# Optimization experiments

Measured on AMD Instinct MI355X. Metric: run time of the kernel, lower is better.

Reference implementation:

```python
import jax, jax.numpy as jnp
import numpy as np

MAT_MODE = [(0, 1), (0, 2), (1, 2)]   # plane axes per component (TensoRF VM)
VEC_MODE = [2, 1, 0]                  # line axis per component
DISTANCE_SCALE = 1.0
WHITE_BG = True


def _bilinear(plane, uv):
    """plane: [C,H,W]; uv: [P,2] in [-1,1] (uv[:,0]->W, uv[:,1]->H). align_corners=True."""
    H, W = plane.shape[-2], plane.shape[-1]
    x = (uv[:, 0] + 1.0) * 0.5 * (W - 1)
    y = (uv[:, 1] + 1.0) * 0.5 * (H - 1)
    x0 = jnp.clip(jnp.floor(x), 0, W - 2).astype(jnp.int32)
    y0 = jnp.clip(jnp.floor(y), 0, H - 2).astype(jnp.int32)
    wx = x - x0
    wy = y - y0
    v00 = plane[:, y0, x0]
    v01 = plane[:, y0, x0 + 1]
    v10 = plane[:, y0 + 1, x0]
    v11 = plane[:, y0 + 1, x0 + 1]
    top = v00 * (1 - wx) + v01 * wx
    bot = v10 * (1 - wx) + v11 * wx
    return top * (1 - wy) + bot * wy   # [C,P]


def _linear1d(line, t):
    """line: [C,L]; t: [P] in [-1,1]. align_corners=True."""
    L = line.shape[-1]
    x = (t + 1.0) * 0.5 * (L - 1)
    x0 = jnp.clip(jnp.floor(x), 0, L - 2).astype(jnp.int32)
    w = x - x0
    return line[:, x0] * (1 - w) + line[:, x0 + 1] * w   # [C,P]


def setup_inputs() -> dict:
    key = jax.random.key(0)
    ks = jax.random.split(key, 8)
    N_rays = 4096
    # camera origins on a sphere of radius 4, dirs aimed at points inside the box
    o = jax.random.normal(ks[0], (N_rays, 3), jnp.float32)
    o = o / jnp.linalg.norm(o, axis=-1, keepdims=True) * 4.0
    tgt = jax.random.uniform(ks[1], (N_rays, 3), jnp.float32, -0.5, 0.5)
    d = tgt - o
    d = d / jnp.linalg.norm(d, axis=-1, keepdims=True)
    rays = jnp.concatenate([o, d], axis=-1)
    return {
        "rays": rays,
        "density_plane": 0.1 * jax.random.normal(ks[2], (3, 16, 256, 256), jnp.float32),
        "density_line": 0.1 * jax.random.normal(ks[3], (3, 16, 256), jnp.float32),
        "app_plane": 0.1 * jax.random.normal(ks[4], (3, 24, 256, 256), jnp.float32),
        "app_line": 0.1 * jax.random.normal(ks[5], (3, 24, 256), jnp.float32),
        "basis_mat": 0.1 * jax.random.normal(ks[6], (72, 3), jnp.float32),
        "aabb": jnp.array([[-1.5, -1.5, -1.5], [1.5, 1.5, 1.5]], jnp.float32),
        "N_samples": 256,
    }


def reference(rays, density_plane, density_line, app_plane, app_line, basis_mat, aabb, N_samples):
    N = rays.shape[0]
    o, d = rays[:, :3], rays[:, 3:6]
    # ray / aabb intersection
    vec = jnp.where(jnp.abs(d) < 1e-6, 1e-6, d)
    rate_a = (aabb[1] - o) / vec
    rate_b = (aabb[0] - o) / vec
    t_min = jnp.clip(jnp.minimum(rate_a, rate_b).max(-1), 0.05)
    t_max = jnp.maximum(jnp.maximum(rate_a, rate_b).min(-1), t_min + 1e-3)
    s = jnp.linspace(0.0, 1.0, N_samples, dtype=jnp.float32)
    z = t_min[:, None] * (1.0 - s) + t_max[:, None] * s          # [N,S]
    dists = jnp.diff(z, axis=-1)
    dists = jnp.concatenate([dists, dists[:, -1:]], axis=-1)      # [N,S]
    pts = o[:, None, :] + d[:, None, :] * z[..., None]            # [N,S,3]
    coords = (pts - aabb[0]) / (aabb[1] - aabb[0]) * 2.0 - 1.0
    inside = jnp.all(jnp.abs(coords) <= 1.0, axis=-1)             # [N,S]
    cf = coords.reshape(-1, 3)                                    # [P,3]

    sigma_feat = 0.0
    app_feats = []
    for i in range(3):
        uv = cf[:, list(MAT_MODE[i])]
        w = cf[:, VEC_MODE[i]]
        sigma_feat = sigma_feat + (_bilinear(density_plane[i], uv) * _linear1d(density_line[i], w)).sum(0)
        app_feats.append(_bilinear(app_plane[i], uv) * _linear1d(app_line[i], w))
    app = jnp.concatenate(app_feats, axis=0).T                    # [P, 72]

    sigma = jax.nn.softplus(sigma_feat).reshape(N, -1) * inside   # [N,S]
    alpha = 1.0 - jnp.exp(-sigma * dists * DISTANCE_SCALE)        # [N,S]
    T = jnp.cumprod(1.0 - alpha + 1e-10, axis=-1)
    T = jnp.concatenate([jnp.ones_like(T[:, :1]), T[:, :-1]], axis=-1)
    weights = alpha * T                                           # [N,S]

    rgb = jax.nn.sigmoid(app @ basis_mat).reshape(N, -1, 3)       # [N,S,3]
    rgb_map = (weights[..., None] * rgb).sum(1)                   # [N,3]
    acc = weights.sum(-1)
    if WHITE_BG:
        rgb_map = rgb_map + (1.0 - acc)[..., None]
    rgb_map = jnp.clip(rgb_map, 0.0, 1.0)
    depth_map = (weights * z).sum(-1, keepdims=True)              # [N,1]
    return rgb_map, depth_map
```

## Files before the change

### kernel.cpp

```cpp
#include <hip/hip_runtime.h>
#include <hip/hip_fp16.h>
#include <cmath>

#define NRAYS 4096
#define NSAMP 256
#define NSAMPLES_TOT (NRAYS * NSAMP)

static constexpr size_t DPT_B = 0;
static constexpr size_t DLT_B = 6291456;
static constexpr size_t APT_B = DLT_B + 24576;
static constexpr size_t ALT_B = APT_B + 6291456;
static constexpr size_t SMP_B = ALT_B + 24576;
static constexpr size_t RAY_B = SMP_B + 8388608;
static constexpr size_t WS_NEED = RAY_B + 131072;

typedef _Float16 __attribute__((ext_vector_type(2))) v2h;
typedef __attribute__((ext_vector_type(2))) float f32x2;

__device__ __forceinline__ float dot2acc(__half2 a, __half2 b, float c) {
  return __builtin_amdgcn_fdot2(__builtin_bit_cast(v2h, a),
                                __builtin_bit_cast(v2h, b), c, false);
}

__device__ __forceinline__ __half2 lerp2(__half2 a, __half2 b, __half2 w) {
  return __hfma2(w, __hsub2(b, a), a);
}

__device__ __forceinline__ void ld8h(const __half* p, __half2 h[4]) {
  uint4 r = *(const uint4*)p;
  h[0] = __builtin_bit_cast(__half2, r.x);
  h[1] = __builtin_bit_cast(__half2, r.y);
  h[2] = __builtin_bit_cast(__half2, r.z);
  h[3] = __builtin_bit_cast(__half2, r.w);
}

__device__ __forceinline__ unsigned pack2h(float a, float b) {
  return __builtin_bit_cast(unsigned, __floats2half2_rn(a, b));
}

__device__ __forceinline__ void dec4f8h(unsigned w, __half2& h0, __half2& h1) {
  f32x2 lo = __builtin_amdgcn_cvt_pk_f32_fp8((int)w, false);
  f32x2 hi = __builtin_amdgcn_cvt_pk_f32_fp8((int)w, true);
  h0 = __floats2half2_rn(lo.x, lo.y);
  h1 = __floats2half2_rn(hi.x, hi.y);
}

__device__ __forceinline__ void dec16f8(uint4 q, __half2 h[8]) {
  dec4f8h(q.x, h[0], h[1]);
  dec4f8h(q.y, h[2], h[3]);
  dec4f8h(q.z, h[4], h[5]);
  dec4f8h(q.w, h[6], h[7]);
}

__device__ __forceinline__ unsigned pk4f8(float a, float b, float c, float d) {
  int w = __builtin_amdgcn_cvt_pk_fp8_f32(a, b, 0, false);
  w = __builtin_amdgcn_cvt_pk_fp8_f32(c, d, w, true);
  return (unsigned)w;
}

__device__ __forceinline__ void grid_uv(float c, int& i0, float& w) {
  float f = (c + 1.0f) * 127.5f;
  float fl = floorf(f);
  fl = fminf(fmaxf(fl, 0.0f), 254.0f);
  i0 = (int)fl;
  w = f - fl;
}

__global__ __launch_bounds__(256) void prep_kernel(
    const float* __restrict__ dp, const float* __restrict__ ap,
    const float* __restrict__ dl, const float* __restrict__ al,
    const float* __restrict__ rays, const float* __restrict__ aabb,
    __half* __restrict__ dpt, unsigned char* __restrict__ apt,
    __half* __restrict__ dlt, unsigned char* __restrict__ alt,
    float4* __restrict__ rd) {
  __shared__ float tile[24][257];
  int b = blockIdx.x, x = threadIdx.x;
  if (b < 768) {
    int i = b >> 8, y = b & 255;
    const float* src = dp + (size_t)(i * 16) * 65536 + y * 256;
#pragma unroll
    for (int c = 0; c < 16; ++c) tile[c][x] = src[c * 65536 + x];
    __syncthreads();
    float f[16];
#pragma unroll
    for (int c = 0; c < 16; ++c) f[c] = tile[c][x];
    uint4 v0, v1;
    v0.x = pack2h(f[0], f[1]);   v0.y = pack2h(f[2], f[3]);
    v0.z = pack2h(f[4], f[5]);   v0.w = pack2h(f[6], f[7]);
    v1.x = pack2h(f[8], f[9]);   v1.y = pack2h(f[10], f[11]);
    v1.z = pack2h(f[12], f[13]); v1.w = pack2h(f[14], f[15]);
    uint4* dst = (uint4*)(dpt + ((size_t)(i << 16) + (y << 8) + x) * 16);
    dst[0] = v0; dst[1] = v1;
  } else if (b < 1536) {
    int t = b - 768;
    int i = t >> 8, y = t & 255;
    const float* src = ap + (size_t)(i * 24) * 65536 + y * 256;
#pragma unroll
    for (int c = 0; c < 24; ++c) tile[c][x] = src[c * 65536 + x];
    __syncthreads();
    float f[24];
#pragma unroll
    for (int c = 0; c < 24; ++c) f[c] = tile[c][x];
    uint4 v0, v1;
    v0.x = pk4f8(f[0], f[1], f[2], f[3]);
    v0.y = pk4f8(f[4], f[5], f[6], f[7]);
    v0.z = pk4f8(f[8], f[9], f[10], f[11]);
    v0.w = pk4f8(f[12], f[13], f[14], f[15]);
    v1.x = pk4f8(f[16], f[17], f[18], f[19]);
    v1.y = pk4f8(f[20], f[21], f[22], f[23]);
    v1.z = 0u; v1.w = 0u;
    uint4* dst = (uint4*)(apt + ((size_t)(i << 16) + (y << 8) + x) * 32);
    dst[0] = v0; dst[1] = v1;
  } else if (b < 1539) {
    int i = b - 1536, l = x;
    float f[16];
#pragma unroll
    for (int c = 0; c < 16; ++c) f[c] = dl[(i * 16 + c) * 256 + l];
    uint4 v0, v1;
    v0.x = pack2h(f[0], f[1]);   v0.y = pack2h(f[2], f[3]);
    v0.z = pack2h(f[4], f[5]);   v0.w = pack2h(f[6], f[7]);
    v1.x = pack2h(f[8], f[9]);   v1.y = pack2h(f[10], f[11]);
    v1.z = pack2h(f[12], f[13]); v1.w = pack2h(f[14], f[15]);
    uint4* dst = (uint4*)(dlt + (i * 256 + l) * 16);
    dst[0] = v0; dst[1] = v1;
  } else if (b < 1542) {
    int i = b - 1539, l = x;
    float f[24];
#pragma unroll
    for (int c = 0; c < 24; ++c) f[c] = al[(i * 24 + c) * 256 + l];
    uint4 v0, v1;
    v0.x = pk4f8(f[0], f[1], f[2], f[3]);
    v0.y = pk4f8(f[4], f[5], f[6], f[7]);
    v0.z = pk4f8(f[8], f[9], f[10], f[11]);
    v0.w = pk4f8(f[12], f[13], f[14], f[15]);
    v1.x = pk4f8(f[16], f[17], f[18], f[19]);
    v1.y = pk4f8(f[20], f[21], f[22], f[23]);
    v1.z = 0u; v1.w = 0u;
    uint4* dst = (uint4*)(alt + (i * 256 + l) * 32);
    dst[0] = v0; dst[1] = v1;
  } else {
    int r = (b - 1542) * 256 + x;
    if (r < NRAYS) {
      float o0 = rays[r * 6 + 0], o1 = rays[r * 6 + 1], o2 = rays[r * 6 + 2];
      float d0 = rays[r * 6 + 3], d1 = rays[r * 6 + 4], d2 = rays[r * 6 + 5];
      float A0 = aabb[0], A1 = aabb[1], A2 = aabb[2];
      float B0 = aabb[3], B1 = aabb[4], B2 = aabb[5];
      float v0 = fabsf(d0) < 1e-6f ? 1e-6f : d0;
      float v1 = fabsf(d1) < 1e-6f ? 1e-6f : d1;
      float v2 = fabsf(d2) < 1e-6f ? 1e-6f : d2;
      float ra0 = (B0 - o0) / v0, rb0 = (A0 - o0) / v0;
      float ra1 = (B1 - o1) / v1, rb1 = (A1 - o1) / v1;
      float ra2 = (B2 - o2) / v2, rb2 = (A2 - o2) / v2;
      float tmin = fmaxf(fmaxf(fminf(ra0, rb0), fminf(ra1, rb1)), fminf(ra2, rb2));
      tmin = fmaxf(tmin, 0.05f);
      float tmax = fminf(fminf(fmaxf(ra0, rb0), fmaxf(ra1, rb1)), fmaxf(ra2, rb2));
      tmax = fmaxf(tmax, tmin + 0.001f);
      float dt = (tmax - tmin) * (1.0f / 255.0f);
      float s0 = 2.0f / (B0 - A0), s1 = 2.0f / (B1 - A1), s2 = 2.0f / (B2 - A2);
      float4 a2, b2;
      a2.x = (o0 - A0) * s0 - 1.0f; a2.y = (o1 - A1) * s1 - 1.0f;
      a2.z = (o2 - A2) * s2 - 1.0f; a2.w = tmin;
      b2.x = d0 * s0; b2.y = d1 * s1; b2.z = d2 * s2; b2.w = dt;
      rd[r * 2] = a2;
      rd[r * 2 + 1] = b2;
    }
  }
}

__device__ __forceinline__ float density_h2(const __half* __restrict__ pl,
                                            const __half* __restrict__ ln,
                                            int x0, __half2 wx, int y0, __half2 wy,
                                            int l0, __half2 wl, int sub,
                                            float acc) {
  const __half* p = pl + ((y0 * 256 + x0) << 4) + sub * 8;
  __half2 v00[4], v01[4], v10[4], v11[4], la[4], lb[4];
  ld8h(p, v00);
  ld8h(p + 16, v01);
  ld8h(p + 4096, v10);
  ld8h(p + 4096 + 16, v11);
  const __half* lp = ln + (l0 << 4) + sub * 8;
  ld8h(lp, la);
  ld8h(lp + 16, lb);
#pragma unroll
  for (int r = 0; r < 4; ++r) {
    __half2 m = lerp2(lerp2(v00[r], v01[r], wx), lerp2(v10[r], v11[r], wx), wy);
    __half2 l = lerp2(la[r], lb[r], wl);
    acc = dot2acc(m, l, acc);
  }
  return acc;
}

__device__ __forceinline__ void app_f8(const unsigned char* __restrict__ pl,
                                       const unsigned char* __restrict__ ln,
                                       const __half2* __restrict__ btR,
                                       const __half2* __restrict__ btG,
                                       const __half2* __restrict__ btB,
                                       int x0, __half2 wx, int y0, __half2 wy,
                                       int l0, __half2 wl, int sub,
                                       float& dr, float& dg, float& db) {
  const unsigned char* p = pl + (size_t)((y0 * 256 + x0) << 5) + sub * 16;
  uint4 qA = *(const uint4*)p;
  uint4 qB = *(const uint4*)(p + 32);
  uint4 qC = *(const uint4*)(p + 8192);
  uint4 qD = *(const uint4*)(p + 8192 + 32);
  const unsigned char* lp = ln + (l0 << 5) + sub * 16;
  uint4 qLA = *(const uint4*)lp;
  uint4 qLB = *(const uint4*)(lp + 32);
  __half2 A[8], B[8], C[8], D[8], LA[8], LB[8];
  dec16f8(qA, A);
  dec16f8(qB, B);
  dec16f8(qC, C);
  dec16f8(qD, D);
  dec16f8(qLA, LA);
  dec16f8(qLB, LB);
#pragma unroll
  for (int r = 0; r < 8; ++r) {
    __half2 m = lerp2(lerp2(A[r], B[r], wx), lerp2(C[r], D[r], wx), wy);
    __half2 l = lerp2(LA[r], LB[r], wl);
    __half2 av = __hmul2(m, l);
    dr = dot2acc(av, btR[r], dr);
    dg = dot2acc(av, btG[r], dg);
    db = dot2acc(av, btB[r], db);
  }
}

__global__ __launch_bounds__(256) void sample_kernel(
    const float4* __restrict__ rd, const float* __restrict__ basis,
    const __half* __restrict__ dpt, const __half* __restrict__ dlt,
    const unsigned char* __restrict__ apt, const unsigned char* __restrict__ alt,
    uint2* __restrict__ smp) {
  __shared__ __align__(16) __half bth[3][3][32];
  int tid = threadIdx.x;
  for (int t = tid; t < 288; t += 256) {
    int k = t / 96, rem = t - k * 96;
    int m = rem >> 5, c = rem & 31;
    float v = (c < 24) ? basis[(m * 24 + c) * 3 + k] : 0.0f;
    bth[k][m][c] = __float2half(v);
  }
  __syncthreads();

  int ray = blockIdx.x >> 1;
  int j = ((blockIdx.x & 1) << 7) + (tid >> 1);
  int sub = tid & 1;

  float4 ra = rd[ray * 2];
  float4 rb = rd[ray * 2 + 1];
  float z = fmaf((float)j, rb.w, ra.w);
  float c0 = fmaf(rb.x, z, ra.x);
  float c1 = fmaf(rb.y, z, ra.y);
  float c2 = fmaf(rb.z, z, ra.z);
  bool inside = (fabsf(c0) <= 1.0f) && (fabsf(c1) <= 1.0f) && (fabsf(c2) <= 1.0f);

  float sig = 0.f, dr = 0.f, dg = 0.f, db = 0.f;
  if (inside) {
    int i0, i1, i2;
    float w0, w1, w2;
    grid_uv(c0, i0, w0);
    grid_uv(c1, i1, w1);
    grid_uv(c2, i2, w2);
    __half2 h0 = __float2half2_rn(w0);
    __half2 h1 = __float2half2_rn(w1);
    __half2 h2 = __float2half2_rn(w2);
    sig = density_h2(dpt + 0 * 1048576, dlt + 0 * 4096, i0, h0, i1, h1, i2, h2, sub, sig);
    sig = density_h2(dpt + 1 * 1048576, dlt + 1 * 4096, i0, h0, i2, h2, i1, h1, sub, sig);
    sig = density_h2(dpt + 2 * 1048576, dlt + 2 * 4096, i1, h1, i2, h2, i0, h0, sub, sig);
    app_f8(apt + 0 * 2097152, alt + 0 * 8192,
           (const __half2*)&bth[0][0][sub * 16], (const __half2*)&bth[1][0][sub * 16],
           (const __half2*)&bth[2][0][sub * 16], i0, h0, i1, h1, i2, h2, sub, dr, dg, db);
    app_f8(apt + 1 * 2097152, alt + 1 * 8192,
           (const __half2*)&bth[0][1][sub * 16], (const __half2*)&bth[1][1][sub * 16],
           (const __half2*)&bth[2][1][sub * 16], i0, h0, i2, h2, i1, h1, sub, dr, dg, db);
    app_f8(apt + 2 * 2097152, alt + 2 * 8192,
           (const __half2*)&bth[0][2][sub * 16], (const __half2*)&bth[1][2][sub * 16],
           (const __half2*)&bth[2][2][sub * 16], i1, h1, i2, h2, i0, h0, sub, dr, dg, db);
  }
  sig += __shfl_xor(sig, 1, 64);
  dr += __shfl_xor(dr, 1, 64);
  dg += __shfl_xor(dg, 1, 64);
  db += __shfl_xor(db, 1, 64);

  if (sub == 0) {
    float sp = fmaxf(sig, 0.f) + log1pf(expf(-fabsf(sig)));
    float alpha = inside ? (1.0f - expf(-sp * rb.w)) : 0.0f;
    float cr = 1.0f / (1.0f + expf(-dr));
    float cg = 1.0f / (1.0f + expf(-dg));
    float cb = 1.0f / (1.0f + expf(-db));
    uint2 sv;
    sv.x = pack2h(alpha, cr);
    sv.y = pack2h(cg, cb);
    smp[ray * 256 + j] = sv;
  }
}

__global__ __launch_bounds__(256) void scan_kernel(
    const float4* __restrict__ rd, const uint2* __restrict__ smp,
    float* __restrict__ out) {
  int tid = threadIdx.x;
  int lane = tid & 63;
  int ray = blockIdx.x * 4 + (tid >> 6);

  float tmin = rd[ray * 2].w;
  float dt = rd[ray * 2 + 1].w;

  float C = 1.0f;
  float racc = 0.f, gacc = 0.f, bacc = 0.f, wsum = 0.f, dsum = 0.f;

  for (int q = 0; q < 4; ++q) {
    int j = q * 64 + lane;
    uint2 sv = smp[ray * 256 + j];
    float2 ar = __half22float2(__builtin_bit_cast(__half2, sv.x));
    float2 gb = __half22float2(__builtin_bit_cast(__half2, sv.y));
    float alpha = ar.x;
    float z = fmaf((float)j, dt, tmin);

    float p = 1.0f - alpha + 1e-10f;
#pragma unroll
    for (int off = 1; off < 64; off <<= 1) {
      float t = __shfl_up(p, off, 64);
      if (lane >= off) p *= t;
    }
    float tot = __shfl(p, 63, 64);
    float e = __shfl_up(p, 1, 64);
    if (lane == 0) e = 1.0f;
    float Tj = C * e;
    float w = alpha * Tj;
    racc += w * ar.y;
    gacc += w * gb.x;
    bacc += w * gb.y;
    wsum += w;
    dsum += w * z;
    C *= tot;
  }

#pragma unroll
  for (int off = 32; off > 0; off >>= 1) {
    racc += __shfl_down(racc, off, 64);
    gacc += __shfl_down(gacc, off, 64);
    bacc += __shfl_down(bacc, off, 64);
    wsum += __shfl_down(wsum, off, 64);
    dsum += __shfl_down(dsum, off, 64);
  }
  if (lane == 0) {
    float bgw = 1.0f - wsum;
    out[ray * 3 + 0] = fminf(fmaxf(racc + bgw, 0.f), 1.f);
    out[ray * 3 + 1] = fminf(fmaxf(gacc + bgw, 0.f), 1.f);
    out[ray * 3 + 2] = fminf(fmaxf(bacc + bgw, 0.f), 1.f);
    out[NRAYS * 3 + ray] = dsum;
  }
}

__device__ __forceinline__ float density_orig(const float* __restrict__ plane,
                                              const float* __restrict__ line,
                                              float cx, float cy, float cw) {
  int x0, y0, l0; float wx, wy, wl;
  grid_uv(cx, x0, wx); grid_uv(cy, y0, wy); grid_uv(cw, l0, wl);
  int base = y0 * 256 + x0;
  float s = 0.0f;
#pragma unroll 4
  for (int c = 0; c < 16; ++c) {
    const float* pc = plane + c * 65536;
    float v00 = pc[base], v01 = pc[base + 1];
    float v10 = pc[base + 256], v11 = pc[base + 257];
    float top = fmaf(wx, v01 - v00, v00);
    float bot = fmaf(wx, v11 - v10, v10);
    float mid = fmaf(wy, bot - top, top);
    float la = line[c * 256 + l0], lb = line[c * 256 + l0 + 1];
    float lv = fmaf(wl, lb - la, la);
    s += mid * lv;
  }
  return s;
}

__device__ __forceinline__ void app_orig(const float* __restrict__ plane,
                                         const float* __restrict__ line,
                                         const float* __restrict__ btR,
                                         const float* __restrict__ btG,
                                         const float* __restrict__ btB,
                                         float cx, float cy, float cw,
                                         float& dr, float& dg, float& db) {
  int x0, y0, l0; float wx, wy, wl;
  grid_uv(cx, x0, wx); grid_uv(cy, y0, wy); grid_uv(cw, l0, wl);
  int base = y0 * 256 + x0;
#pragma unroll 4
  for (int c = 0; c < 24; ++c) {
    const float* pc = plane + c * 65536;
    float v00 = pc[base], v01 = pc[base + 1];
    float v10 = pc[base + 256], v11 = pc[base + 257];
    float top = fmaf(wx, v01 - v00, v00);
    float bot = fmaf(wx, v11 - v10, v10);
    float mid = fmaf(wy, bot - top, top);
    float la = line[c * 256 + l0], lb = line[c * 256 + l0 + 1];
    float lv = fmaf(wl, lb - la, la);
    float av = mid * lv;
    dr += av * btR[c]; dg += av * btG[c]; db += av * btB[c];
  }
}

__global__ __launch_bounds__(256) void render_fallback(
    const float* __restrict__ rays, const float* __restrict__ basis,
    const float* __restrict__ aabb, const float* __restrict__ dplane,
    const float* __restrict__ dline, const float* __restrict__ aplane,
    const float* __restrict__ aline, float* __restrict__ out) {
  __shared__ float bt[3 * 72];
  int tid = threadIdx.x;
  if (tid < 216) {
    int k = tid / 72, r = tid - k * 72;
    bt[tid] = basis[r * 3 + k];
  }
  __syncthreads();
  int lane = tid & 63;
  int ray = blockIdx.x * 4 + (tid >> 6);

  float o0 = rays[ray * 6 + 0], o1 = rays[ray * 6 + 1], o2 = rays[ray * 6 + 2];
  float d0 = rays[ray * 6 + 3], d1 = rays[ray * 6 + 4], d2 = rays[ray * 6 + 5];
  float A0 = aabb[0], A1 = aabb[1], A2 = aabb[2];
  float B0 = aabb[3], B1 = aabb[4], B2 = aabb[5];
  float v0 = fabsf(d0) < 1e-6f ? 1e-6f : d0;
  float v1 = fabsf(d1) < 1e-6f ? 1e-6f : d1;
  float v2 = fabsf(d2) < 1e-6f ? 1e-6f : d2;
  float ra0 = (B0 - o0) / v0, rb0 = (A0 - o0) / v0;
  float ra1 = (B1 - o1) / v1, rb1 = (A1 - o1) / v1;
  float ra2 = (B2 - o2) / v2, rb2 = (A2 - o2) / v2;
  float tmin = fmaxf(fmaxf(fminf(ra0, rb0), fminf(ra1, rb1)), fminf(ra2, rb2));
  tmin = fmaxf(tmin, 0.05f);
  float tmax = fminf(fminf(fmaxf(ra0, rb0), fmaxf(ra1, rb1)), fmaxf(ra2, rb2));
  tmax = fmaxf(tmax, tmin + 0.001f);
  float dt = (tmax - tmin) * (1.0f / 255.0f);
  float s0 = 2.0f / (B0 - A0), s1 = 2.0f / (B1 - A1), s2 = 2.0f / (B2 - A2);

  float C = 1.0f;
  float racc = 0.f, gacc = 0.f, bacc = 0.f, wsum = 0.f, dsum = 0.f;
  for (int q = 0; q < 4; ++q) {
    int j = q * 64 + lane;
    float sfrac = (float)j * (1.0f / 255.0f);
    float z = tmin * (1.0f - sfrac) + tmax * sfrac;
    float c0 = (o0 + d0 * z - A0) * s0 - 1.0f;
    float c1 = (o1 + d1 * z - A1) * s1 - 1.0f;
    float c2 = (o2 + d2 * z - A2) * s2 - 1.0f;
    bool inside = (fabsf(c0) <= 1.0f) && (fabsf(c1) <= 1.0f) && (fabsf(c2) <= 1.0f);
    float alpha = 0.f, cr = 0.f, cg = 0.f, cb = 0.f;
    if (inside) {
      float sig = 0.f, dr = 0.f, dg = 0.f, db = 0.f;
      sig += density_orig(dplane + 0 * 1048576, dline + 0 * 4096, c0, c1, c2);
      sig += density_orig(dplane + 1 * 1048576, dline + 1 * 4096, c0, c2, c1);
      sig += density_orig(dplane + 2 * 1048576, dline + 2 * 4096, c1, c2, c0);
      app_orig(aplane + 0 * 1572864, aline + 0 * 6144,
               &bt[0 * 72 + 0], &bt[1 * 72 + 0], &bt[2 * 72 + 0],
               c0, c1, c2, dr, dg, db);
      app_orig(aplane + 1 * 1572864, aline + 1 * 6144,
               &bt[0 * 72 + 24], &bt[1 * 72 + 24], &bt[2 * 72 + 24],
               c0, c2, c1, dr, dg, db);
      app_orig(aplane + 2 * 1572864, aline + 2 * 6144,
               &bt[0 * 72 + 48], &bt[1 * 72 + 48], &bt[2 * 72 + 48],
               c1, c2, c0, dr, dg, db);
      float sp = fmaxf(sig, 0.f) + log1pf(expf(-fabsf(sig)));
      alpha = 1.0f - expf(-sp * dt);
      cr = 1.0f / (1.0f + expf(-dr));
      cg = 1.0f / (1.0f + expf(-dg));
      cb = 1.0f / (1.0f + expf(-db));
    }
    float p = 1.0f - alpha + 1e-10f;
#pragma unroll
    for (int off = 1; off < 64; off <<= 1) {
      float t = __shfl_up(p, off, 64);
      if (lane >= off) p *= t;
    }
    float tot = __shfl(p, 63, 64);
    float e = __shfl_up(p, 1, 64);
    if (lane == 0) e = 1.0f;
    float Tj = C * e;
    float w = alpha * Tj;
    racc += w * cr; gacc += w * cg; bacc += w * cb;
    wsum += w; dsum += w * z;
    C *= tot;
  }
#pragma unroll
  for (int off = 32; off > 0; off >>= 1) {
    racc += __shfl_down(racc, off, 64);
    gacc += __shfl_down(gacc, off, 64);
    bacc += __shfl_down(bacc, off, 64);
    wsum += __shfl_down(wsum, off, 64);
    dsum += __shfl_down(dsum, off, 64);
  }
  if (lane == 0) {
    float bgw = 1.0f - wsum;
    out[ray * 3 + 0] = fminf(fmaxf(racc + bgw, 0.f), 1.f);
    out[ray * 3 + 1] = fminf(fmaxf(gacc + bgw, 0.f), 1.f);
    out[ray * 3 + 2] = fminf(fmaxf(bacc + bgw, 0.f), 1.f);
    out[NRAYS * 3 + ray] = dsum;
  }
}

extern "C" void kernel_launch(void* const* d_in, const int* in_sizes, int n_in,
                              void* d_out, int out_size, void* d_ws, size_t ws_size,
                              hipStream_t stream) {
  const float* rays  = (const float*)d_in[0];
  const float* dp    = (const float*)d_in[1];
  const float* dl    = (const float*)d_in[2];
  const float* ap    = (const float*)d_in[3];
  const float* al    = (const float*)d_in[4];
  const float* basis = (const float*)d_in[5];
  const float* aabb  = (const float*)d_in[6];
  float* out = (float*)d_out;

  if (ws_size >= WS_NEED) {
    char* ws = (char*)d_ws;
    __half* dpt = (__half*)(ws + DPT_B);
    __half* dlt = (__half*)(ws + DLT_B);
    unsigned char* apt = (unsigned char*)(ws + APT_B);
    unsigned char* alt = (unsigned char*)(ws + ALT_B);
    uint2* smp = (uint2*)(ws + SMP_B);
    float4* rayd = (float4*)(ws + RAY_B);
    prep_kernel<<<1558, 256, 0, stream>>>(dp, ap, dl, al, rays, aabb,
                                          dpt, apt, dlt, alt, rayd);
    sample_kernel<<<NRAYS * 2, 256, 0, stream>>>(rayd, basis, dpt, dlt, apt, alt, smp);
    scan_kernel<<<NRAYS / 4, 256, 0, stream>>>(rayd, smp, out);
  } else {
    render_fallback<<<NRAYS / 4, 256, 0, stream>>>(
        rays, basis, aabb, dp, dl, ap, al, out);
  }
}
```

Measured before the change: 171.2 us.

## Store density planes in fp8, drop app padding, precompute bilinear weights

Density plane tables are quantized from fp16 to fp8, which halves their footprint. Appearance plane and line tables are packed at 24 bytes per texel instead of a padded 32, cutting the gather bytes per sample. Bilinear interpolation now uses four precomputed corner weights per plane, each shared by the density and appearance lookups, instead of nested lerps. In exchange the density features lose precision, and the 12-byte unaligned loads may split into several smaller memory instructions.

```diff
diff --git a/kernel.cpp b/kernel.cpp
--- a/kernel.cpp
+++ b/kernel.cpp
@@ -7,15 +7,23 @@
 #define NSAMPLES_TOT (NRAYS * NSAMP)
 
 static constexpr size_t DPT_B = 0;
-static constexpr size_t DLT_B = 6291456;
+static constexpr size_t DLT_B = 3145728;
 static constexpr size_t APT_B = DLT_B + 24576;
-static constexpr size_t ALT_B = APT_B + 6291456;
-static constexpr size_t SMP_B = ALT_B + 24576;
+static constexpr size_t ALT_B = APT_B + 4718592;
+static constexpr size_t SMP_B = ALT_B + 18432;
 static constexpr size_t RAY_B = SMP_B + 8388608;
 static constexpr size_t WS_NEED = RAY_B + 131072;
 
 typedef _Float16 __attribute__((ext_vector_type(2))) v2h;
 typedef __attribute__((ext_vector_type(2))) float f32x2;
+
+struct u96 { unsigned x, y, z; };
+
+__device__ __forceinline__ u96 ld12(const void* p) {
+  u96 v;
+  __builtin_memcpy(&v, p, 12);
+  return v;
+}
 
 __device__ __forceinline__ float dot2acc(__half2 a, __half2 b, float c) {
   return __builtin_amdgcn_fdot2(__builtin_bit_cast(v2h, a),
@@ -45,11 +53,15 @@
   h1 = __floats2half2_rn(hi.x, hi.y);
 }
 
-__device__ __forceinline__ void dec16f8(uint4 q, __half2 h[8]) {
+__device__ __forceinline__ void dec8f8(uint2 q, __half2 h[4]) {
+  dec4f8h(q.x, h[0], h[1]);
+  dec4f8h(q.y, h[2], h[3]);
+}
+
+__device__ __forceinline__ void dec12f8(u96 q, __half2 h[6]) {
   dec4f8h(q.x, h[0], h[1]);
   dec4f8h(q.y, h[2], h[3]);
   dec4f8h(q.z, h[4], h[5]);
-  dec4f8h(q.w, h[6], h[7]);
 }
 
 __device__ __forceinline__ unsigned pk4f8(float a, float b, float c, float d) {
@@ -66,11 +78,20 @@
   w = f - fl;
 }
 
+__device__ __forceinline__ void bilin_w(float wx, float wy, __half2& W00,
+                                        __half2& W01, __half2& W10, __half2& W11) {
+  float ix = 1.0f - wx, iy = 1.0f - wy;
+  W00 = __float2half2_rn(ix * iy);
+  W01 = __float2half2_rn(wx * iy);
+  W10 = __float2half2_rn(ix * wy);
+  W11 = __float2half2_rn(wx * wy);
+}
+
 __global__ __launch_bounds__(256) void prep_kernel(
     const float* __restrict__ dp, const float* __restrict__ ap,
     const float* __restrict__ dl, const float* __restrict__ al,
     const float* __restrict__ rays, const float* __restrict__ aabb,
-    __half* __restrict__ dpt, unsigned char* __restrict__ apt,
+    unsigned char* __restrict__ dpt, unsigned char* __restrict__ apt,
     __half* __restrict__ dlt, unsigned char* __restrict__ alt,
     float4* __restrict__ rd) {
   __shared__ float tile[24][257];
@@ -84,13 +105,12 @@
     float f[16];
 #pragma unroll
     for (int c = 0; c < 16; ++c) f[c] = tile[c][x];
-    uint4 v0, v1;
-    v0.x = pack2h(f[0], f[1]);   v0.y = pack2h(f[2], f[3]);
-    v0.z = pack2h(f[4], f[5]);   v0.w = pack2h(f[6], f[7]);
-    v1.x = pack2h(f[8], f[9]);   v1.y = pack2h(f[10], f[11]);
-    v1.z = pack2h(f[12], f[13]); v1.w = pack2h(f[14], f[15]);
-    uint4* dst = (uint4*)(dpt + ((size_t)(i << 16) + (y << 8) + x) * 16);
-    dst[0] = v0; dst[1] = v1;
+    uint4 v;
+    v.x = pk4f8(f[0], f[1], f[2], f[3]);
+    v.y = pk4f8(f[4], f[5], f[6], f[7]);
+    v.z = pk4f8(f[8], f[9], f[10], f[11]);
+    v.w = pk4f8(f[12], f[13], f[14], f[15]);
+    *(uint4*)(dpt + ((size_t)(i << 16) + (y << 8) + x) * 16) = v;
   } else if (b < 1536) {
     int t = b - 768;
     int i = t >> 8, y = t & 255;
@@ -101,16 +121,10 @@
     float f[24];
 #pragma unroll
     for (int c = 0; c < 24; ++c) f[c] = tile[c][x];
-    uint4 v0, v1;
-    v0.x = pk4f8(f[0], f[1], f[2], f[3]);
-    v0.y = pk4f8(f[4], f[5], f[6], f[7]);
-    v0.z = pk4f8(f[8], f[9], f[10], f[11]);
-    v0.w = pk4f8(f[12], f[13], f[14], f[15]);
-    v1.x = pk4f8(f[16], f[17], f[18], f[19]);
-    v1.y = pk4f8(f[20], f[21], f[22], f[23]);
-    v1.z = 0u; v1.w = 0u;
-    uint4* dst = (uint4*)(apt + ((size_t)(i << 16) + (y << 8) + x) * 32);
-    dst[0] = v0; dst[1] = v1;
+    unsigned* dst = (unsigned*)(apt + ((size_t)(i << 16) + (y << 8) + x) * 24);
+#pragma unroll
+    for (int k = 0; k < 6; ++k)
+      dst[k] = pk4f8(f[k * 4], f[k * 4 + 1], f[k * 4 + 2], f[k * 4 + 3]);
   } else if (b < 1539) {
     int i = b - 1536, l = x;
     float f[16];
@@ -128,16 +142,10 @@
     float f[24];
 #pragma unroll
     for (int c = 0; c < 24; ++c) f[c] = al[(i * 24 + c) * 256 + l];
-    uint4 v0, v1;
-    v0.x = pk4f8(f[0], f[1], f[2], f[3]);
-    v0.y = pk4f8(f[4], f[5], f[6], f[7]);
-    v0.z = pk4f8(f[8], f[9], f[10], f[11]);
-    v0.w = pk4f8(f[12], f[13], f[14], f[15]);
-    v1.x = pk4f8(f[16], f[17], f[18], f[19]);
-    v1.y = pk4f8(f[20], f[21], f[22], f[23]);
-    v1.z = 0u; v1.w = 0u;
-    uint4* dst = (uint4*)(alt + (i * 256 + l) * 32);
-    dst[0] = v0; dst[1] = v1;
+    unsigned* dst = (unsigned*)(alt + (i * 256 + l) * 24);
+#pragma unroll
+    for (int k = 0; k < 6; ++k)
+      dst[k] = pk4f8(f[k * 4], f[k * 4 + 1], f[k * 4 + 2], f[k * 4 + 3]);
   } else {
     int r = (b - 1542) * 256 + x;
     if (r < NRAYS) {
@@ -167,23 +175,27 @@
   }
 }
 
-__device__ __forceinline__ float density_h2(const __half* __restrict__ pl,
+__device__ __forceinline__ float density_f8(const unsigned char* __restrict__ pl,
                                             const __half* __restrict__ ln,
-                                            int x0, __half2 wx, int y0, __half2 wy,
-                                            int l0, __half2 wl, int sub,
-                                            float acc) {
-  const __half* p = pl + ((y0 * 256 + x0) << 4) + sub * 8;
-  __half2 v00[4], v01[4], v10[4], v11[4], la[4], lb[4];
-  ld8h(p, v00);
-  ld8h(p + 16, v01);
-  ld8h(p + 4096, v10);
-  ld8h(p + 4096 + 16, v11);
+                                            int x0, int y0, int l0,
+                                            __half2 W00, __half2 W01,
+                                            __half2 W10, __half2 W11,
+                                            __half2 wl, int sub, float acc) {
+  const unsigned char* p = pl + (size_t)((y0 * 256 + x0) << 4) + sub * 8;
+  uint2 q00 = *(const uint2*)p;
+  uint2 q01 = *(const uint2*)(p + 16);
+  uint2 q10 = *(const uint2*)(p + 4096);
+  uint2 q11 = *(const uint2*)(p + 4096 + 16);
+  __half2 A[4], B[4], C[4], D[4], la[4], lb[4];
+  dec8f8(q00, A); dec8f8(q01, B); dec8f8(q10, C); dec8f8(q11, D);
   const __half* lp = ln + (l0 << 4) + sub * 8;
-  ld8h(lp, la);
-  ld8h(lp + 16, lb);
+  ld8h(lp, la); ld8h(lp + 16, lb);
 #pragma unroll
   for (int r = 0; r < 4; ++r) {
-    __half2 m = lerp2(lerp2(v00[r], v01[r], wx), lerp2(v10[r], v11[r], wx), wy);
+    __half2 m = __hmul2(W00, A[r]);
+    m = __hfma2(W01, B[r], m);
+    m = __hfma2(W10, C[r], m);
+    m = __hfma2(W11, D[r], m);
     __half2 l = lerp2(la[r], lb[r], wl);
     acc = dot2acc(m, l, acc);
   }
@@ -195,27 +207,28 @@
                                        const __half2* __restrict__ btR,
                                        const __half2* __restrict__ btG,
                                        const __half2* __restrict__ btB,
-                                       int x0, __half2 wx, int y0, __half2 wy,
-                                       int l0, __half2 wl, int sub,
+                                       int x0, int y0, int l0,
+                                       __half2 W00, __half2 W01,
+                                       __half2 W10, __half2 W11,
+                                       __half2 wl, int sub,
                                        float& dr, float& dg, float& db) {
-  const unsigned char* p = pl + (size_t)((y0 * 256 + x0) << 5) + sub * 16;
-  uint4 qA = *(const uint4*)p;
-  uint4 qB = *(const uint4*)(p + 32);
-  uint4 qC = *(const uint4*)(p + 8192);
-  uint4 qD = *(const uint4*)(p + 8192 + 32);
-  const unsigned char* lp = ln + (l0 << 5) + sub * 16;
-  uint4 qLA = *(const uint4*)lp;
-  uint4 qLB = *(const uint4*)(lp + 32);
-  __half2 A[8], B[8], C[8], D[8], LA[8], LB[8];
-  dec16f8(qA, A);
-  dec16f8(qB, B);
-  dec16f8(qC, C);
-  dec16f8(qD, D);
-  dec16f8(qLA, LA);
-  dec16f8(qLB, LB);
-#pragma unroll
-  for (int r = 0; r < 8; ++r) {
-    __half2 m = lerp2(lerp2(A[r], B[r], wx), lerp2(C[r], D[r], wx), wy);
+  const unsigned char* p = pl + (size_t)(y0 * 256 + x0) * 24 + sub * 12;
+  u96 qA = ld12(p);
+  u96 qB = ld12(p + 24);
+  u96 qC = ld12(p + 6144);
+  u96 qD = ld12(p + 6144 + 24);
+  const unsigned char* lp = ln + l0 * 24 + sub * 12;
+  u96 qLA = ld12(lp);
+  u96 qLB = ld12(lp + 24);
+  __half2 A[6], B[6], C[6], D[6], LA[6], LB[6];
+  dec12f8(qA, A); dec12f8(qB, B); dec12f8(qC, C); dec12f8(qD, D);
+  dec12f8(qLA, LA); dec12f8(qLB, LB);
+#pragma unroll
+  for (int r = 0; r < 6; ++r) {
+    __half2 m = __hmul2(W00, A[r]);
+    m = __hfma2(W01, B[r], m);
+    m = __hfma2(W10, C[r], m);
+    m = __hfma2(W11, D[r], m);
     __half2 l = lerp2(LA[r], LB[r], wl);
     __half2 av = __hmul2(m, l);
     dr = dot2acc(av, btR[r], dr);
@@ -226,16 +239,15 @@
 
 __global__ __launch_bounds__(256) void sample_kernel(
     const float4* __restrict__ rd, const float* __restrict__ basis,
-    const __half* __restrict__ dpt, const __half* __restrict__ dlt,
+    const unsigned char* __restrict__ dpt, const __half* __restrict__ dlt,
     const unsigned char* __restrict__ apt, const unsigned char* __restrict__ alt,
     uint2* __restrict__ smp) {
-  __shared__ __align__(16) __half bth[3][3][32];
+  __shared__ __align__(16) __half bth[3][3][24];
   int tid = threadIdx.x;
-  for (int t = tid; t < 288; t += 256) {
-    int k = t / 96, rem = t - k * 96;
-    int m = rem >> 5, c = rem & 31;
-    float v = (c < 24) ? basis[(m * 24 + c) * 3 + k] : 0.0f;
-    bth[k][m][c] = __float2half(v);
+  if (tid < 216) {
+    int k = tid / 72, rem = tid - k * 72;
+    int m = rem / 24, c = rem - m * 24;
+    bth[k][m][c] = __float2half(basis[(m * 24 + c) * 3 + k]);
   }
   __syncthreads();
 
@@ -261,18 +273,31 @@
     __half2 h0 = __float2half2_rn(w0);
     __half2 h1 = __float2half2_rn(w1);
     __half2 h2 = __float2half2_rn(w2);
-    sig = density_h2(dpt + 0 * 1048576, dlt + 0 * 4096, i0, h0, i1, h1, i2, h2, sub, sig);
-    sig = density_h2(dpt + 1 * 1048576, dlt + 1 * 4096, i0, h0, i2, h2, i1, h1, sub, sig);
-    sig = density_h2(dpt + 2 * 1048576, dlt + 2 * 4096, i1, h1, i2, h2, i0, h0, sub, sig);
-    app_f8(apt + 0 * 2097152, alt + 0 * 8192,
-           (const __half2*)&bth[0][0][sub * 16], (const __half2*)&bth[1][0][sub * 16],
-           (const __half2*)&bth[2][0][sub * 16], i0, h0, i1, h1, i2, h2, sub, dr, dg, db);
-    app_f8(apt + 1 * 2097152, alt + 1 * 8192,
-           (const __half2*)&bth[0][1][sub * 16], (const __half2*)&bth[1][1][sub * 16],
-           (const __half2*)&bth[2][1][sub * 16], i0, h0, i2, h2, i1, h1, sub, dr, dg, db);
-    app_f8(apt + 2 * 2097152, alt + 2 * 8192,
-           (const __half2*)&bth[0][2][sub * 16], (const __half2*)&bth[1][2][sub * 16],
-           (const __half2*)&bth[2][2][sub * 16], i1, h1, i2, h2, i0, h0, sub, dr, dg, db);
+    __half2 Wa00, Wa01, Wa10, Wa11;
+    __half2 Wb00, Wb01, Wb10, Wb11;
+    __half2 Wc00, Wc01, Wc10, Wc11;
+    bilin_w(w0, w1, Wa00, Wa01, Wa10, Wa11);
+    bilin_w(w0, w2, Wb00, Wb01, Wb10, Wb11);
+    bilin_w(w1, w2, Wc00, Wc01, Wc10, Wc11);
+
+    sig = density_f8(dpt + 0 * 1048576, dlt + 0 * 4096, i0, i1, i2,
+                     Wa00, Wa01, Wa10, Wa11, h2, sub, sig);
+    sig = density_f8(dpt + 1 * 1048576, dlt + 1 * 4096, i0, i2, i1,
+                     Wb00, Wb01, Wb10, Wb11, h1, sub, sig);
+    sig = density_f8(dpt + 2 * 1048576, dlt + 2 * 4096, i1, i2, i0,
+                     Wc00, Wc01, Wc10, Wc11, h0, sub, sig);
+    app_f8(apt + 0 * 1572864, alt + 0 * 6144,
+           (const __half2*)&bth[0][0][sub * 12], (const __half2*)&bth[1][0][sub * 12],
+           (const __half2*)&bth[2][0][sub * 12], i0, i1, i2,
+           Wa00, Wa01, Wa10, Wa11, h2, sub, dr, dg, db);
+    app_f8(apt + 1 * 1572864, alt + 1 * 6144,
+           (const __half2*)&bth[0][1][sub * 12], (const __half2*)&bth[1][1][sub * 12],
+           (const __half2*)&bth[2][1][sub * 12], i0, i2, i1,
+           Wb00, Wb01, Wb10, Wb11, h1, sub, dr, dg, db);
+    app_f8(apt + 2 * 1572864, alt + 2 * 6144,
+           (const __half2*)&bth[0][2][sub * 12], (const __half2*)&bth[1][2][sub * 12],
+           (const __half2*)&bth[2][2][sub * 12], i1, i2, i0,
+           Wc00, Wc01, Wc10, Wc11, h0, sub, dr, dg, db);
   }
   sig += __shfl_xor(sig, 1, 64);
   dr += __shfl_xor(dr, 1, 64);
@@ -505,7 +530,7 @@
 
   if (ws_size >= WS_NEED) {
     char* ws = (char*)d_ws;
-    __half* dpt = (__half*)(ws + DPT_B);
+    unsigned char* dpt = (unsigned char*)(ws + DPT_B);
     __half* dlt = (__half*)(ws + DLT_B);
     unsigned char* apt = (unsigned char*)(ws + APT_B);
     unsigned char* alt = (unsigned char*)(ws + ALT_B);
```

After: 165.2 us. -3.5%, faster.
